# Kernel tuning notes

Measured on AMD Instinct MI355X. Metric: run time of the kernel, lower is better.

## Reference

```python
import jax, jax.numpy as jnp
import numpy as np

B, C, Q, E = 32, 1024, 64, 256  # batch, max_context_len, max_question_len, embedding_size
FE = 4 * E                      # final_encoding_size (self_attention=False)


def setup_inputs() -> dict:
    key = jax.random.key(0)
    ks = jax.random.split(key, 7)
    return {
        "context": jax.random.normal(ks[0], (B, C, E), dtype=jnp.float32),
        "question": jax.random.normal(ks[1], (B, Q, E), dtype=jnp.float32),
        "context_mask": jnp.ones((B, C), dtype=jnp.float32),
        "w_question": jax.random.normal(ks[2], (E,), dtype=jnp.float32),
        "w_context": jax.random.normal(ks[3], (E,), dtype=jnp.float32),
        "w_multiple": jax.random.normal(ks[4], (E,), dtype=jnp.float32),
        "final_W": jax.random.normal(ks[5], (FE, FE), dtype=jnp.float32) * (1.0 / np.sqrt(FE)),
        "final_b": jnp.zeros((FE,), dtype=jnp.float32),
    }


def reference(context, question, context_mask, w_question, w_context, w_multiple, final_W, final_b):
    # Trilinear similarity: s[b,c,q] = <w_q, q_q> + <w_c, c_c> + <w_m, c_c * q_q>
    q_weighted = question @ w_question                 # (B, Q)
    ctx_weighted = context @ w_context                 # (B, C)
    # (question.unsqueeze(1) * context.unsqueeze(2)) @ w_multiple, computed
    # without materializing the (B, C, Q, E) intermediate:
    mult = jnp.einsum('bce,bqe->bcq', context * w_multiple, question)  # (B, C, Q)
    similarity = ctx_weighted[:, :, None] + q_weighted[:, None, :] + mult  # (B, C, Q)

    # Context-to-query attention (softmax over question dim)
    c2q_att = jnp.einsum('bcq,bqe->bce', jax.nn.softmax(similarity, axis=2), question)

    # Query-to-context attention (softmax over context dim of row-max scores)
    q2c_weights = jax.nn.softmax(jnp.max(similarity, axis=2), axis=1)   # (B, C)
    q2c_att = jnp.einsum('bc,bce->be', q2c_weights, context)            # (B, E)

    attended = jnp.concatenate(
        [context, c2q_att, context * c2q_att, context * q2c_att[:, None, :]],
        axis=2)                                                          # (B, C, 4E)

    # MaskedLinear: affine map, output rows zeroed where context_mask == 0
    out = (attended @ final_W.T + final_b) * context_mask[:, :, None]    # (B, C, 4E)
    return out
```

## Files before the change

### kernel.cpp

```cpp
#include <hip/hip_runtime.h>

#define BB 32
#define CC 1024
#define QQ 64
#define EE 256
#define FE 1024
#define MM (BB*CC)

typedef __bf16 bf16_t;
typedef bf16_t bf16x8 __attribute__((ext_vector_type(8)));
typedef float f32x4 __attribute__((ext_vector_type(4)));

__device__ __forceinline__ unsigned short f2bf(float f) {
  unsigned u = __float_as_uint(f);
  u += 0x7fffu + ((u >> 16) & 1u);
  return (unsigned short)(u >> 16);
}
__device__ __forceinline__ float bf2f(unsigned short u) {
  return __uint_as_float(((unsigned)u) << 16);
}

__device__ __forceinline__ void gload_lds16(const void* g, void* l) {
  __builtin_amdgcn_global_load_lds(
      (const __attribute__((address_space(1))) unsigned int*)g,
      (__attribute__((address_space(3))) unsigned int*)l, 16, 0, 0);
}

__global__ void k_prep_q(const float* __restrict__ question, const float* __restrict__ w_question,
                         const float* __restrict__ w_multiple, float* __restrict__ qm,
                         float* __restrict__ qw) {
  int gid = blockIdx.x * 256 + threadIdx.x;
  int row = gid >> 6;
  int lane = gid & 63;
  const float4 q = *(const float4*)(question + (size_t)row * EE + lane * 4);
  const float4 wm = *(const float4*)(w_multiple + lane * 4);
  const float4 wq = *(const float4*)(w_question + lane * 4);
  float4 r; r.x = q.x*wm.x; r.y = q.y*wm.y; r.z = q.z*wm.z; r.w = q.w*wm.w;
  *(float4*)(qm + (size_t)row * EE + lane * 4) = r;
  float d = q.x*wq.x + q.y*wq.y + q.z*wq.z + q.w*wq.w;
  d += __shfl_xor(d, 1);  d += __shfl_xor(d, 2);  d += __shfl_xor(d, 4);
  d += __shfl_xor(d, 8);  d += __shfl_xor(d, 16); d += __shfl_xor(d, 32);
  if (lane == 0) qw[row] = d;
}

__global__ void k_cast_w(const float* __restrict__ W, unsigned short* __restrict__ Wb) {
  int i = (blockIdx.x * 256 + threadIdx.x) * 4;
  float4 v = *(const float4*)(W + i);
  ushort4 o; o.x = f2bf(v.x); o.y = f2bf(v.y); o.z = f2bf(v.z); o.w = f2bf(v.w);
  *(ushort4*)(Wb + i) = o;
}

#define DOT4(acc, A, Bv) acc += A.x*Bv.x + A.y*Bv.y + A.z*Bv.z + A.w*Bv.w

__launch_bounds__(256)
__global__ void k_sim(const float* __restrict__ ctx, const float* __restrict__ qm,
                      const float* __restrict__ qw_g, const float* __restrict__ w_context,
                      float* __restrict__ P, float* __restrict__ rowmax,
                      unsigned short* __restrict__ att) {
  __shared__ float qml[QQ][260];
  __shared__ float ck[64][36];
  __shared__ float cwl[64];
  __shared__ float qwl[QQ];
  const int tid = threadIdx.x;
  const int b = blockIdx.y;
  const int c0 = blockIdx.x * 64;
  const int tx = tid & 15, ty = tid >> 4;

  const float* qmb = qm + (size_t)b * (QQ * EE);
  for (int idx = tid * 4; idx < QQ * EE; idx += 1024) {
    float4 v = *(const float4*)(qmb + idx);
    *(float4*)&qml[idx >> 8][idx & 255] = v;
  }
  if (tid < QQ) qwl[tid] = qw_g[b * QQ + tid];

  const int cr = tid >> 3, er = (tid & 7) * 4;
  const float* crow0 = ctx + ((size_t)(b * CC + c0 + cr)) * EE;
  const float* crow1 = crow0 + 32 * EE;
  unsigned short* arow0 = att + ((size_t)(b * CC + c0 + cr)) * FE;
  unsigned short* arow1 = arow0 + (size_t)32 * FE;
  float s[4][4] = {{0.f}};
  float cp0 = 0.f, cp1 = 0.f;

  for (int eo = 0; eo < EE; eo += 32) {
    float4 cv0 = *(const float4*)(crow0 + eo + er);
    float4 cv1 = *(const float4*)(crow1 + eo + er);
    float4 wc = *(const float4*)(w_context + eo + er);
    cp0 += cv0.x*wc.x + cv0.y*wc.y + cv0.z*wc.z + cv0.w*wc.w;
    cp1 += cv1.x*wc.x + cv1.y*wc.y + cv1.z*wc.z + cv1.w*wc.w;
    ushort4 u0, u1;
    u0.x = f2bf(cv0.x); u0.y = f2bf(cv0.y); u0.z = f2bf(cv0.z); u0.w = f2bf(cv0.w);
    u1.x = f2bf(cv1.x); u1.y = f2bf(cv1.y); u1.z = f2bf(cv1.z); u1.w = f2bf(cv1.w);
    *(ushort4*)(arow0 + eo + er) = u0;
    *(ushort4*)(arow1 + eo + er) = u1;
    __syncthreads();
    *(float4*)&ck[cr][er] = cv0;
    *(float4*)&ck[cr + 32][er] = cv1;
    __syncthreads();
#pragma unroll
    for (int ee = 0; ee < 32; ee += 4) {
      float4 a0 = *(const float4*)&ck[ty +  0][ee];
      float4 a1 = *(const float4*)&ck[ty + 16][ee];
      float4 a2 = *(const float4*)&ck[ty + 32][ee];
      float4 a3 = *(const float4*)&ck[ty + 48][ee];
      float4 b0 = *(const float4*)&qml[tx +  0][eo + ee];
      float4 b1 = *(const float4*)&qml[tx + 16][eo + ee];
      float4 b2 = *(const float4*)&qml[tx + 32][eo + ee];
      float4 b3 = *(const float4*)&qml[tx + 48][eo + ee];
      DOT4(s[0][0], a0, b0); DOT4(s[0][1], a0, b1); DOT4(s[0][2], a0, b2); DOT4(s[0][3], a0, b3);
      DOT4(s[1][0], a1, b0); DOT4(s[1][1], a1, b1); DOT4(s[1][2], a1, b2); DOT4(s[1][3], a1, b3);
      DOT4(s[2][0], a2, b0); DOT4(s[2][1], a2, b1); DOT4(s[2][2], a2, b2); DOT4(s[2][3], a2, b3);
      DOT4(s[3][0], a3, b0); DOT4(s[3][1], a3, b1); DOT4(s[3][2], a3, b2); DOT4(s[3][3], a3, b3);
    }
  }
  cp0 += __shfl_xor(cp0, 1); cp0 += __shfl_xor(cp0, 2); cp0 += __shfl_xor(cp0, 4);
  cp1 += __shfl_xor(cp1, 1); cp1 += __shfl_xor(cp1, 2); cp1 += __shfl_xor(cp1, 4);
  if ((tid & 7) == 0) { cwl[cr] = cp0; cwl[cr + 32] = cp1; }
  __syncthreads();

#pragma unroll
  for (int i = 0; i < 4; ++i) {
    int c = ty + 16 * i;
    float cw = cwl[c];
    float f[4], mx = -1e30f;
#pragma unroll
    for (int j = 0; j < 4; ++j) {
      f[j] = s[i][j] + cw + qwl[tx + 16 * j];
      mx = fmaxf(mx, f[j]);
    }
    mx = fmaxf(mx, __shfl_xor(mx, 1));
    mx = fmaxf(mx, __shfl_xor(mx, 2));
    mx = fmaxf(mx, __shfl_xor(mx, 4));
    mx = fmaxf(mx, __shfl_xor(mx, 8));
    float sum = 0.f;
#pragma unroll
    for (int j = 0; j < 4; ++j) { f[j] = expf(f[j] - mx); sum += f[j]; }
    sum += __shfl_xor(sum, 1);
    sum += __shfl_xor(sum, 2);
    sum += __shfl_xor(sum, 4);
    sum += __shfl_xor(sum, 8);
    float inv = 1.f / sum;
    if (tx == 0) rowmax[(size_t)b * CC + c0 + c] = mx;
    size_t prow = ((size_t)(b * CC + c0 + c)) * QQ;
#pragma unroll
    for (int j = 0; j < 4; ++j) P[prow + tx + 16 * j] = f[j] * inv;
  }
}

__global__ void k_q2c_softmax(const float* __restrict__ rowmax, float* __restrict__ q2cw) {
  int b = blockIdx.x, tid = threadIdx.x;
  __shared__ float rbuf[4], sbuf[4];
  float4 v = *(const float4*)(rowmax + (size_t)b * CC + tid * 4);
  float m = fmaxf(fmaxf(v.x, v.y), fmaxf(v.z, v.w));
  for (int off = 1; off < 64; off <<= 1) m = fmaxf(m, __shfl_xor(m, off));
  int wv = tid >> 6;
  if ((tid & 63) == 0) rbuf[wv] = m;
  __syncthreads();
  m = fmaxf(fmaxf(rbuf[0], rbuf[1]), fmaxf(rbuf[2], rbuf[3]));
  float e0 = expf(v.x - m), e1 = expf(v.y - m), e2 = expf(v.z - m), e3 = expf(v.w - m);
  float sum = e0 + e1 + e2 + e3;
  for (int off = 1; off < 64; off <<= 1) sum += __shfl_xor(sum, off);
  if ((tid & 63) == 0) sbuf[wv] = sum;
  __syncthreads();
  sum = sbuf[0] + sbuf[1] + sbuf[2] + sbuf[3];
  float inv = 1.f / sum;
  float4 o; o.x = e0 * inv; o.y = e1 * inv; o.z = e2 * inv; o.w = e3 * inv;
  *(float4*)(q2cw + (size_t)b * CC + tid * 4) = o;
}

__global__ void k_q2c_part(const unsigned short* __restrict__ att, const float* __restrict__ w,
                           float* __restrict__ part) {
  int b = blockIdx.y, ch = blockIdx.x;
  int e = threadIdx.x;
  const unsigned short* base = att + ((size_t)(b * CC + ch * 128)) * FE + e;
  const float* wp = w + b * CC + ch * 128;
  float acc = 0.f;
#pragma unroll 4
  for (int c = 0; c < 128; ++c) acc += wp[c] * bf2f(base[(size_t)c * FE]);
  part[(b * 8 + ch) * EE + e] = acc;
}

__global__ void k_q2c_sum(const float* __restrict__ part, float* __restrict__ q2catt) {
  int b = blockIdx.x, e = threadIdx.x;
  float a = 0.f;
#pragma unroll
  for (int ch = 0; ch < 8; ++ch) a += part[(b * 8 + ch) * EE + e];
  q2catt[b * EE + e] = a;
}

__launch_bounds__(256)
__global__ void k_pv(const float* __restrict__ P, const float* __restrict__ question,
                     const float* __restrict__ q2catt, unsigned short* __restrict__ attended) {
  __shared__ float PT[QQ][65];
  __shared__ float ql[QQ][68];
  const int tid = threadIdx.x;
  const int b = blockIdx.y, c0 = blockIdx.x * 64;
  const int tx = tid & 15, ty = tid >> 4;

  {
    int q4 = (tid & 15) * 4, cb = tid >> 4;
#pragma unroll
    for (int r = 0; r < 4; ++r) {
      int c = cb + 16 * r;
      float4 v = *(const float4*)(P + ((size_t)(b * CC + c0 + c)) * QQ + q4);
      PT[q4 + 0][c] = v.x; PT[q4 + 1][c] = v.y; PT[q4 + 2][c] = v.z; PT[q4 + 3][c] = v.w;
    }
  }
  const float* qb = question + (size_t)b * (QQ * EE);
  const float* g2 = q2catt + b * EE;

  for (int ep = 0; ep < EE; ep += 64) {
    __syncthreads();
    {
      int q = tid >> 2, e16 = (tid & 3) * 16;
      const float* src = qb + (size_t)q * EE + ep + e16;
      float4 v0 = *(const float4*)(src);
      float4 v1 = *(const float4*)(src + 4);
      float4 v2 = *(const float4*)(src + 8);
      float4 v3 = *(const float4*)(src + 12);
      *(float4*)&ql[q][e16]      = v0;
      *(float4*)&ql[q][e16 + 4]  = v1;
      *(float4*)&ql[q][e16 + 8]  = v2;
      *(float4*)&ql[q][e16 + 12] = v3;
    }
    __syncthreads();
    float s[4][4] = {{0.f}};
#pragma unroll 8
    for (int q = 0; q < QQ; ++q) {
      float a0 = PT[q][ty];
      float a1 = PT[q][ty + 16];
      float a2 = PT[q][ty + 32];
      float a3 = PT[q][ty + 48];
      float4 bv = *(const float4*)&ql[q][tx * 4];
      s[0][0] += a0 * bv.x; s[0][1] += a0 * bv.y; s[0][2] += a0 * bv.z; s[0][3] += a0 * bv.w;
      s[1][0] += a1 * bv.x; s[1][1] += a1 * bv.y; s[1][2] += a1 * bv.z; s[1][3] += a1 * bv.w;
      s[2][0] += a2 * bv.x; s[2][1] += a2 * bv.y; s[2][2] += a2 * bv.z; s[2][3] += a2 * bv.w;
      s[3][0] += a3 * bv.x; s[3][1] += a3 * bv.y; s[3][2] += a3 * bv.z; s[3][3] += a3 * bv.w;
    }
    float4 gv = *(const float4*)(g2 + ep + tx * 4);
#pragma unroll
    for (int i = 0; i < 4; ++i) {
      int c = ty + 16 * i;
      size_t row = (size_t)(b * CC + c0 + c);
      unsigned short* arow = attended + row * (size_t)FE;
      ushort4 cu = *(const ushort4*)(arow + 0 * EE + ep + tx * 4);
      float cx = bf2f(cu.x), cy = bf2f(cu.y), cz = bf2f(cu.z), cw = bf2f(cu.w);
      ushort4 s1, s2, s3;
      s1.x = f2bf(s[i][0]);        s1.y = f2bf(s[i][1]);        s1.z = f2bf(s[i][2]);        s1.w = f2bf(s[i][3]);
      s2.x = f2bf(cx * s[i][0]);   s2.y = f2bf(cy * s[i][1]);   s2.z = f2bf(cz * s[i][2]);   s2.w = f2bf(cw * s[i][3]);
      s3.x = f2bf(cx * gv.x);      s3.y = f2bf(cy * gv.y);      s3.z = f2bf(cz * gv.z);      s3.w = f2bf(cw * gv.w);
      *(ushort4*)(arow + 1 * EE + ep + tx * 4) = s1;
      *(ushort4*)(arow + 2 * EE + ep + tx * 4) = s2;
      *(ushort4*)(arow + 3 * EE + ep + tx * 4) = s3;
    }
  }
}

__launch_bounds__(256)
__global__ void k_gemm(const unsigned short* __restrict__ A, const unsigned short* __restrict__ Bw,
                       const float* __restrict__ bias, const float* __restrict__ mask,
                       float* __restrict__ out) {
  __shared__ bf16_t As[2][128][64];
  __shared__ bf16_t Bs[2][128][64];
  const int tid = threadIdx.x;
  const int lane = tid & 63;
  const int wave = tid >> 6;
  const int wr = wave >> 1, wc = wave & 1;

  const int bid = blockIdx.x;
  const int wg = (bid & 7) * 256 + (bid >> 3);
  const int bcol = (wg & 7) * 128;
  const int brow = (wg >> 3) * 128;

  const int r = lane & 15, kg = lane >> 4;

  const int rr = tid >> 3;
  const int sl = tid & 7;
  const int srcslot = (sl ^ (rr & 7)) * 8;
  const unsigned short* ga0 = A  + (size_t)(brow + rr) * FE + srcslot;
  const unsigned short* gb0 = Bw + (size_t)(bcol + rr) * FE + srcslot;

  f32x4 acc[4][4] = {};

#define STAGE(bufi, t)                                                        \
  {                                                                           \
    const int k0 = (t) * 64;                                                  \
    _Pragma("unroll")                                                         \
    for (int r0 = 0; r0 < 128; r0 += 32) {                                    \
      gload_lds16(ga0 + (size_t)r0 * FE + k0, &As[bufi][r0 + rr][sl * 8]);    \
      gload_lds16(gb0 + (size_t)r0 * FE + k0, &Bs[bufi][r0 + rr][sl * 8]);    \
    }                                                                         \
  }

  STAGE(0, 0);
  __syncthreads();

  for (int t = 0; t < 16; ++t) {
    const int cur = t & 1;
    if (t < 15) STAGE(cur ^ 1, t + 1);

    bf16x8 fa[4][2], fb[4][2];
#pragma unroll
    for (int m = 0; m < 4; ++m) {
      const int rowa = wr * 64 + m * 16 + r;
      const int key = rowa & 7;
#pragma unroll
      for (int ks = 0; ks < 2; ++ks)
        fa[m][ks] = *(const bf16x8*)&As[cur][rowa][((ks * 4 + kg) ^ key) * 8];
    }
#pragma unroll
    for (int n = 0; n < 4; ++n) {
      const int rowb = wc * 64 + n * 16 + r;
      const int key = rowb & 7;
#pragma unroll
      for (int ks = 0; ks < 2; ++ks)
        fb[n][ks] = *(const bf16x8*)&Bs[cur][rowb][((ks * 4 + kg) ^ key) * 8];
    }
#pragma unroll
    for (int ks = 0; ks < 2; ++ks)
#pragma unroll
      for (int m = 0; m < 4; ++m)
#pragma unroll
        for (int n = 0; n < 4; ++n)
          acc[m][n] = __builtin_amdgcn_mfma_f32_16x16x32_bf16(fa[m][ks], fb[n][ks], acc[m][n], 0, 0, 0);

    if (t < 15) __syncthreads();
  }
#undef STAGE

#pragma unroll
  for (int m = 0; m < 4; ++m) {
#pragma unroll
    for (int n = 0; n < 4; ++n) {
#pragma unroll
      for (int reg = 0; reg < 4; ++reg) {
        int row = brow + wr * 64 + m * 16 + kg * 4 + reg;
        int col = bcol + wc * 64 + n * 16 + r;
        out[(size_t)row * FE + col] = (acc[m][n][reg] + bias[col]) * mask[row];
      }
    }
  }
}

extern "C" void kernel_launch(void* const* d_in, const int* in_sizes, int n_in,
                              void* d_out, int out_size, void* d_ws, size_t ws_size,
                              hipStream_t stream) {
  const float* ctx  = (const float*)d_in[0];
  const float* ques = (const float*)d_in[1];
  const float* mask = (const float*)d_in[2];
  const float* w_q  = (const float*)d_in[3];
  const float* w_c  = (const float*)d_in[4];
  const float* w_m  = (const float*)d_in[5];
  const float* fW   = (const float*)d_in[6];
  const float* fb   = (const float*)d_in[7];
  float* out = (float*)d_out;

  char* ws = (char*)d_ws;
  float* qm     = (float*)(ws);
  float* qw     = (float*)(ws + 8388608);
  float* rowmax = (float*)(ws + 8396800);
  float* q2cw   = (float*)(ws + 8527872);
  float* part   = (float*)(ws + 8658944);
  float* q2catt = (float*)(ws + 8921088);
  float* P      = (float*)(ws + 8953856);
  unsigned short* attended = (unsigned short*)(ws + 17342464);
  unsigned short* Wb       = (unsigned short*)(ws + 84451328);

  k_prep_q<<<512, 256, 0, stream>>>(ques, w_q, w_m, qm, qw);
  k_cast_w<<<1024, 256, 0, stream>>>(fW, Wb);
  k_sim<<<dim3(16, 32), 256, 0, stream>>>(ctx, qm, qw, w_c, P, rowmax, attended);
  k_q2c_softmax<<<32, 256, 0, stream>>>(rowmax, q2cw);
  k_q2c_part<<<dim3(8, 32), 256, 0, stream>>>(attended, q2cw, part);
  k_q2c_sum<<<32, 256, 0, stream>>>(part, q2catt);
  k_pv<<<dim3(16, 32), 256, 0, stream>>>(P, ques, q2catt, attended);
  k_gemm<<<2048, 256, 0, stream>>>(attended, Wb, fb, mask, out);
}
```

Before: 189.3 us.

## Enlarge GEMM tile to 256x256 with 8 waves and deeper prefetch pipeline

The final GEMM moves from 128x128 tiles with 4 waves to 256x256 tiles with 8 waves per block, so each wave computes 128x64 outputs. The aim is more data reuse from LDS and fewer global loads per FLOP. The global-to-LDS loads are now issued two stages ahead and gated by explicit vmcnt waits with raw s_barriers instead of __syncthreads. MFMA priority is raised with s_setprio. The cost is 128 KB of LDS per block and only 512 blocks, which lowers occupancy and risks a tail effect.

```diff
diff --git a/kernel.cpp b/kernel.cpp
--- a/kernel.cpp
+++ b/kernel.cpp
@@ -255,85 +255,96 @@
   }
 }
 
-__launch_bounds__(256)
+__launch_bounds__(512, 2)
 __global__ void k_gemm(const unsigned short* __restrict__ A, const unsigned short* __restrict__ Bw,
                        const float* __restrict__ bias, const float* __restrict__ mask,
                        float* __restrict__ out) {
-  __shared__ bf16_t As[2][128][64];
-  __shared__ bf16_t Bs[2][128][64];
+  __shared__ bf16_t As[2][256][64];
+  __shared__ bf16_t Bs[2][256][64];
   const int tid = threadIdx.x;
   const int lane = tid & 63;
   const int wave = tid >> 6;
-  const int wr = wave >> 1, wc = wave & 1;
+  const int wr = wave >> 2;
+  const int wc = wave & 3;
 
   const int bid = blockIdx.x;
-  const int wg = (bid & 7) * 256 + (bid >> 3);
-  const int bcol = (wg & 7) * 128;
-  const int brow = (wg >> 3) * 128;
-
-  const int r = lane & 15, kg = lane >> 4;
-
-  const int rr = tid >> 3;
-  const int sl = tid & 7;
-  const int srcslot = (sl ^ (rr & 7)) * 8;
-  const unsigned short* ga0 = A  + (size_t)(brow + rr) * FE + srcslot;
-  const unsigned short* gb0 = Bw + (size_t)(bcol + rr) * FE + srcslot;
-
-  f32x4 acc[4][4] = {};
-
-#define STAGE(bufi, t)                                                        \
-  {                                                                           \
-    const int k0 = (t) * 64;                                                  \
-    _Pragma("unroll")                                                         \
-    for (int r0 = 0; r0 < 128; r0 += 32) {                                    \
-      gload_lds16(ga0 + (size_t)r0 * FE + k0, &As[bufi][r0 + rr][sl * 8]);    \
-      gload_lds16(gb0 + (size_t)r0 * FE + k0, &Bs[bufi][r0 + rr][sl * 8]);    \
-    }                                                                         \
+  const int wg = (bid & 7) * 64 + (bid >> 3);
+  const int brow = (wg >> 2) * 256;
+  const int bcol = (wg & 3) * 256;
+
+  const int r = lane & 15, kg4 = lane >> 4;
+  const int lxor = lane & 7;
+
+  const int srow = tid >> 3;
+  const int sg = (tid & 7) ^ (srow & 7);
+  const unsigned short* gA = A  + (size_t)(brow + srow) * FE + sg * 8;
+  const unsigned short* gB = Bw + (size_t)(bcol + srow) * FE + sg * 8;
+  bf16_t* ldsA = &As[0][srow][(tid & 7) * 8];
+  bf16_t* ldsB = &Bs[0][srow][(tid & 7) * 8];
+
+  f32x4 acc[8][4] = {};
+
+#define STAGE(bufi, t)                                                          \
+  {                                                                             \
+    const int k0 = (t) * 64;                                                    \
+    _Pragma("unroll")                                                           \
+    for (int r0 = 0; r0 < 256; r0 += 64) {                                      \
+      gload_lds16(gA + (size_t)r0 * FE + k0, ldsA + (size_t)(bufi) * (256*64) + r0 * 64); \
+      gload_lds16(gB + (size_t)r0 * FE + k0, ldsB + (size_t)(bufi) * (256*64) + r0 * 64); \
+    }                                                                           \
   }
 
   STAGE(0, 0);
-  __syncthreads();
+  STAGE(1, 1);
 
   for (int t = 0; t < 16; ++t) {
     const int cur = t & 1;
-    if (t < 15) STAGE(cur ^ 1, t + 1);
-
-    bf16x8 fa[4][2], fb[4][2];
-#pragma unroll
-    for (int m = 0; m < 4; ++m) {
-      const int rowa = wr * 64 + m * 16 + r;
-      const int key = rowa & 7;
+    if (t < 15) {
+      asm volatile("s_waitcnt vmcnt(8)" ::: "memory");
+    } else {
+      asm volatile("s_waitcnt vmcnt(0)" ::: "memory");
+    }
+    __builtin_amdgcn_s_barrier();
+
+    bf16x8 fa[8][2], fb[4][2];
+#pragma unroll
+    for (int m = 0; m < 8; ++m) {
+      const int rowa = wr * 128 + m * 16 + r;
 #pragma unroll
       for (int ks = 0; ks < 2; ++ks)
-        fa[m][ks] = *(const bf16x8*)&As[cur][rowa][((ks * 4 + kg) ^ key) * 8];
+        fa[m][ks] = *(const bf16x8*)&As[cur][rowa][((ks * 4 + kg4) ^ lxor) * 8];
     }
 #pragma unroll
     for (int n = 0; n < 4; ++n) {
       const int rowb = wc * 64 + n * 16 + r;
-      const int key = rowb & 7;
 #pragma unroll
       for (int ks = 0; ks < 2; ++ks)
-        fb[n][ks] = *(const bf16x8*)&Bs[cur][rowb][((ks * 4 + kg) ^ key) * 8];
-    }
+        fb[n][ks] = *(const bf16x8*)&Bs[cur][rowb][((ks * 4 + kg4) ^ lxor) * 8];
+    }
+    asm volatile("s_waitcnt lgkmcnt(0)" ::: "memory");
+    __builtin_amdgcn_s_barrier();
+
+    if (t < 14) STAGE(cur, t + 2);
+
+    __builtin_amdgcn_s_setprio(1);
 #pragma unroll
     for (int ks = 0; ks < 2; ++ks)
 #pragma unroll
-      for (int m = 0; m < 4; ++m)
+      for (int m = 0; m < 8; ++m)
 #pragma unroll
         for (int n = 0; n < 4; ++n)
           acc[m][n] = __builtin_amdgcn_mfma_f32_16x16x32_bf16(fa[m][ks], fb[n][ks], acc[m][n], 0, 0, 0);
-
-    if (t < 15) __syncthreads();
+    __builtin_amdgcn_s_setprio(0);
   }
 #undef STAGE
 
 #pragma unroll
-  for (int m = 0; m < 4; ++m) {
+  for (int m = 0; m < 8; ++m) {
 #pragma unroll
     for (int n = 0; n < 4; ++n) {
 #pragma unroll
       for (int reg = 0; reg < 4; ++reg) {
-        int row = brow + wr * 64 + m * 16 + kg * 4 + reg;
+        int row = brow + wr * 128 + m * 16 + kg4 * 4 + reg;
         int col = bcol + wc * 64 + n * 16 + r;
         out[(size_t)row * FE + col] = (acc[m][n][reg] + bias[col]) * mask[row];
       }
@@ -372,5 +383,5 @@
   k_q2c_part<<<dim3(8, 32), 256, 0, stream>>>(attended, q2cw, part);
   k_q2c_sum<<<32, 256, 0, stream>>>(part, q2catt);
   k_pv<<<dim3(16, 32), 256, 0, stream>>>(P, ques, q2catt, attended);
-  k_gemm<<<2048, 256, 0, stream>>>(attended, Wb, fb, mask, out);
-}
+  k_gemm<<<512, 512, 0, stream>>>(attended, Wb, fb, mask, out);
+}
```

After: 178.5 us. 5.7% less time.
